# Performance work log

Measured on AMD Instinct MI355X. Metric: run time of the kernel, lower is better.

The kernel has to match this reference:

```python
import jax, jax.numpy as jnp
import numpy as np

N_NODES = 100000
N_EDGES = 1600000
IN = 128
HID = 128
EPS = 1e-5


def setup_inputs() -> dict:
    key = jax.random.key(0)
    ks = jax.random.split(key, 20)
    def lin(k, fi, fo):
        return jax.random.normal(k, (fi, fo), dtype=jnp.float32) / np.sqrt(fi)
    inp = {
        'x': jax.random.normal(ks[0], (N_NODES, IN), dtype=jnp.float32),
        'src': jax.random.randint(ks[1], (N_EDGES,), 0, N_NODES),
        'dst': jax.random.randint(ks[2], (N_EDGES,), 0, N_NODES),
        # SAGEConv layer 1..3: fc_self, fc_neigh, bias
        'Wself1': lin(ks[3], IN, HID), 'Wneigh1': lin(ks[4], IN, HID), 'b1': jnp.zeros((HID,), jnp.float32),
        'Wself2': lin(ks[5], HID, HID), 'Wneigh2': lin(ks[6], HID, HID), 'b2': jnp.zeros((HID,), jnp.float32),
        'Wself3': lin(ks[7], HID, HID), 'Wneigh3': lin(ks[8], HID, HID), 'b3': jnp.zeros((HID,), jnp.float32),
        # shared BatchNorm1d(hid)
        'gamma': jnp.ones((HID,), jnp.float32), 'beta': jnp.zeros((HID,), jnp.float32),
        # decoder MLP hid->hid->hid->1
        'Wd1': lin(ks[9], HID, HID), 'bd1': jnp.zeros((HID,), jnp.float32),
        'Wd2': lin(ks[10], HID, HID), 'bd2': jnp.zeros((HID,), jnp.float32),
        'Wd3': lin(ks[11], HID, 1), 'bd3': jnp.zeros((1,), jnp.float32),
    }
    return inp


def _sage_conv(h, src, dst, deg, Wself, Wneigh, b, n):
    # mean aggregation over in-neighbors: gather + segment-sum + divide
    neigh_sum = jax.ops.segment_sum(h[src], dst, num_segments=n)  # [N, F]
    neigh_mean = neigh_sum / deg[:, None]
    return h @ Wself + neigh_mean @ Wneigh + b


def _batch_norm(h, gamma, beta):
    mu = jnp.mean(h, axis=0)
    var = jnp.mean(jnp.square(h - mu), axis=0)  # biased var, as torch BN training
    return gamma * (h - mu) * jax.lax.rsqrt(var + EPS) + beta


def reference(x, src, dst, Wself1, Wneigh1, b1, Wself2, Wneigh2, b2,
              Wself3, Wneigh3, b3, gamma, beta, Wd1, bd1, Wd2, bd2, Wd3, bd3):
    n = x.shape[0]
    deg = jax.ops.segment_sum(jnp.ones_like(dst, dtype=x.dtype), dst, num_segments=n)
    deg = jnp.maximum(deg, 1.0)
    h = _sage_conv(x, src, dst, deg, Wself1, Wneigh1, b1, n)
    h = jax.nn.relu(_batch_norm(h, gamma, beta))  # dropout = identity (eval)
    h = _sage_conv(h, src, dst, deg, Wself2, Wneigh2, b2, n)
    h = jax.nn.relu(_batch_norm(h, gamma, beta))
    h = _sage_conv(h, src, dst, deg, Wself3, Wneigh3, b3, n)
    # decoder MLP
    h = jax.nn.relu(h @ Wd1 + bd1)
    h = jax.nn.relu(h @ Wd2 + bd2)
    return h @ Wd3 + bd3  # [N, 1]
```

## Files before the change

### kernel.cpp

```cpp
#include <hip/hip_runtime.h>

typedef unsigned short u16;
typedef unsigned int u32;
using bf16x8 = __attribute__((ext_vector_type(8))) __bf16;
using f32x4  = __attribute__((ext_vector_type(4))) float;

#define CAP 48

__global__ void SAGE_79328045957727_kernel() {}

__device__ __forceinline__ float bf2f(u16 u) {
  union { u32 i; float f; } v; v.i = ((u32)u) << 16; return v.f;
}
__device__ __forceinline__ u16 f2bf(float f) {
  union { float f; u32 i; } v; v.f = f;
  u32 x = v.i;
  return (u16)((x + 0x7FFFu + ((x >> 16) & 1u)) >> 16);
}


__global__ void zero_kernel(int* p, int n) {
  int i = blockIdx.x * 256 + threadIdx.x;
  if (i < n) p[i] = 0;
}


__global__ __launch_bounds__(256) void build_kernel(
    const int* __restrict__ src, const int* __restrict__ dst,
    int* __restrict__ deg, int* __restrict__ csr, int E, int npart,
    const float* __restrict__ x, u16* __restrict__ xb, long nelem4,
    const float* w0, const float* w1, const float* w2, const float* w3,
    const float* w4, const float* w5, const float* w6, const float* w7,
    u16* __restrict__ wt) {
  int b = blockIdx.x;
  if (b < 1024) {
    int p = b & 7;
    int brank = b >> 3;
    int lo = p * npart, hi = lo + npart;
    for (int i = brank * 256 + threadIdx.x; i < E; i += 128 * 256) {
      int dv = dst[i];
      if (dv >= lo && dv < hi) {
        int pos = atomicAdd(&deg[dv], 1);
        if (pos < CAP) csr[(size_t)dv * CAP + pos] = src[i];
      }
    }
  } else if (b < 1280) {
    long t = (long)(b - 1024) * 256 + threadIdx.x;
    for (long i4 = t; i4 < nelem4; i4 += 256 * 256) {
      float4 v = ((const float4*)x)[i4];
      u32* op = (u32*)(xb + i4 * 4);
      op[0] = ((u32)f2bf(v.y) << 16) | (u32)f2bf(v.x);
      op[1] = ((u32)f2bf(v.w) << 16) | (u32)f2bf(v.z);
    }
  } else {
    int tg = (b - 1280) * 256 + threadIdx.x;
    for (int k = 0; k < 8; ++k) {
      int idx = tg + k * 16384;
      int m = idx >> 14;
      int i = idx & 16383;
      const float* W = m == 0 ? w0 : m == 1 ? w1 : m == 2 ? w2 : m == 3 ? w3
                     : m == 4 ? w4 : m == 5 ? w5 : m == 6 ? w6 : w7;
      int r = i >> 7, c = i & 127;
      wt[(size_t)m * 16384 + (size_t)c * 128 + r] = f2bf(W[i]);
    }
  }
}


template <int BNIN>
__global__ __launch_bounds__(256) void gather_mean_kernel(
    const u16* __restrict__ H, const int* __restrict__ csr,
    const int* __restrict__ deg, const float* __restrict__ stats,
    const float* __restrict__ gamma, const float* __restrict__ beta,
    u16* __restrict__ M, int N, float invN) {
  __shared__ float sSc[128], sSh[128];
  if (BNIN) {
    int t = threadIdx.x;
    if (t < 128) {
      float mu = stats[t] * invN;
      float var = stats[128 + t] * invN - mu * mu;
      float is = rsqrtf(var + 1e-5f);
      float sc = gamma[t] * is;
      sSc[t] = sc;
      sSh[t] = beta[t] - mu * sc;
    }
    __syncthreads();
  }
  int node = blockIdx.x * 16 + (threadIdx.x >> 4);
  if (node >= N) return;
  int lane = threadIdx.x & 15;
  int fo = lane * 8;
  float sc[8], sh[8];
  if (BNIN) {
    for (int j = 0; j < 8; ++j) { sc[j] = sSc[fo + j]; sh[j] = sSh[fo + j]; }
  }
  const int* nl = csr + (size_t)node * CAP;
  int d = deg[node];
  int dm = d < CAP ? d : CAP;
  float a0=0.f,a1=0.f,a2=0.f,a3=0.f,a4=0.f,a5=0.f,a6=0.f,a7=0.f;

#define ACCQ(q) do { \
    float e0 = bf2f((u16)((q).x & 0xffffu)), e1 = bf2f((u16)((q).x >> 16)); \
    float e2 = bf2f((u16)((q).y & 0xffffu)), e3 = bf2f((u16)((q).y >> 16)); \
    float e4 = bf2f((u16)((q).z & 0xffffu)), e5 = bf2f((u16)((q).z >> 16)); \
    float e6 = bf2f((u16)((q).w & 0xffffu)), e7 = bf2f((u16)((q).w >> 16)); \
    if (BNIN) { \
      e0 = fmaxf(sc[0]*e0+sh[0], 0.f); e1 = fmaxf(sc[1]*e1+sh[1], 0.f); \
      e2 = fmaxf(sc[2]*e2+sh[2], 0.f); e3 = fmaxf(sc[3]*e3+sh[3], 0.f); \
      e4 = fmaxf(sc[4]*e4+sh[4], 0.f); e5 = fmaxf(sc[5]*e5+sh[5], 0.f); \
      e6 = fmaxf(sc[6]*e6+sh[6], 0.f); e7 = fmaxf(sc[7]*e7+sh[7], 0.f); \
    } \
    a0 += e0; a1 += e1; a2 += e2; a3 += e3; \
    a4 += e4; a5 += e5; a6 += e6; a7 += e7; \
  } while (0)

  int e = 0;
  for (; e + 4 <= dm; e += 4) {
    int i0 = nl[e], i1 = nl[e + 1], i2 = nl[e + 2], i3 = nl[e + 3];
    uint4 q0 = *(const uint4*)(H + (size_t)i0 * 128 + fo);
    uint4 q1 = *(const uint4*)(H + (size_t)i1 * 128 + fo);
    uint4 q2 = *(const uint4*)(H + (size_t)i2 * 128 + fo);
    uint4 q3 = *(const uint4*)(H + (size_t)i3 * 128 + fo);
    ACCQ(q0); ACCQ(q1); ACCQ(q2); ACCQ(q3);
  }
  for (; e < dm; ++e) {
    uint4 q = *(const uint4*)(H + (size_t)nl[e] * 128 + fo);
    ACCQ(q);
  }
#undef ACCQ
  float inv = 1.f / (float)(d > 0 ? d : 1);
  uint4 o;
  o.x = ((u32)f2bf(a1 * inv) << 16) | (u32)f2bf(a0 * inv);
  o.y = ((u32)f2bf(a3 * inv) << 16) | (u32)f2bf(a2 * inv);
  o.z = ((u32)f2bf(a5 * inv) << 16) | (u32)f2bf(a4 * inv);
  o.w = ((u32)f2bf(a7 * inv) << 16) | (u32)f2bf(a6 * inv);
  *(uint4*)(M + (size_t)node * 128 + fo) = o;
}


#define LDSROW 136

template <int DUAL, int RELU, int STATS, int BNIN, int FINAL>
__global__ __launch_bounds__(256) void gemm_mfma(
    const u16* __restrict__ A, const u16* __restrict__ B,
    const u16* __restrict__ W1t, const u16* __restrict__ W2t,
    const float* __restrict__ bias, u16* __restrict__ C,
    float* __restrict__ statsOut, const float* __restrict__ statsIn,
    const float* __restrict__ gamma, const float* __restrict__ beta,
    const float* __restrict__ wd3, const float* __restrict__ bd3,
    float* __restrict__ outF, int N, float invN) {
  __shared__ u16 sT[128 * LDSROW];
  __shared__ float sSc[128], sSh[128];
  __shared__ float sOut[128];

  int tid = threadIdx.x;
  int wave = tid >> 6;
  int lane = tid & 63;
  int l15 = lane & 15;
  int quad = lane >> 4;
  size_t row0 = (size_t)blockIdx.x * 128;

  if (BNIN || FINAL) {
    if (tid < 128) {
      if (BNIN) {
        float mu = statsIn[tid] * invN;
        float var = statsIn[128 + tid] * invN - mu * mu;
        float is = rsqrtf(var + 1e-5f);
        float sc = gamma[tid] * is;
        sSc[tid] = sc;
        sSh[tid] = beta[tid] - mu * sc;
      }
      if (FINAL) sOut[tid] = 0.f;
    }
    __syncthreads();
  }

  float bsc[8], bsh[8];
  int cbase = ((tid * 4) & 63) * 2;
  if (BNIN) {
    for (int j = 0; j < 8; ++j) { bsc[j] = sSc[cbase + j]; bsh[j] = sSh[cbase + j]; }
  }

  f32x4 acc[8][2];
  for (int rt = 0; rt < 8; ++rt)
    for (int ct = 0; ct < 2; ++ct)
      for (int i = 0; i < 4; ++i) acc[rt][ct][i] = 0.f;

  bf16x8 wf[2][4];

  for (int ph = 0; ph < (DUAL ? 2 : 1); ++ph) {
    const u16* Asrc = ph ? B : A;
    const u16* Wt = ph ? W2t : W1t;

    for (int ct = 0; ct < 2; ++ct) {
      int col = wave * 32 + ct * 16 + l15;
      for (int kk = 0; kk < 4; ++kk)
        wf[ct][kk] = *(const bf16x8*)(Wt + (size_t)col * 128 + kk * 32 + quad * 8);
    }

    if (ph) __syncthreads();
    for (int j = 0; j < 8; ++j) {
      int idx = j * 1024 + tid * 4;
      int r = idx >> 6;
      int c = idx & 63;
      size_t grow = row0 + r;
      if (grow >= (size_t)N) grow = (size_t)(N - 1);
      const u32* gp = (const u32*)(Asrc + grow * 128) + c;
      u32 v0 = gp[0], v1 = gp[1], v2 = gp[2], v3 = gp[3];
      if (BNIN && ph == 0) {
        float e0 = fmaxf(bsc[0]*bf2f((u16)(v0 & 0xffffu))+bsh[0], 0.f);
        float e1 = fmaxf(bsc[1]*bf2f((u16)(v0 >> 16))+bsh[1], 0.f);
        float e2 = fmaxf(bsc[2]*bf2f((u16)(v1 & 0xffffu))+bsh[2], 0.f);
        float e3 = fmaxf(bsc[3]*bf2f((u16)(v1 >> 16))+bsh[3], 0.f);
        float e4 = fmaxf(bsc[4]*bf2f((u16)(v2 & 0xffffu))+bsh[4], 0.f);
        float e5 = fmaxf(bsc[5]*bf2f((u16)(v2 >> 16))+bsh[5], 0.f);
        float e6 = fmaxf(bsc[6]*bf2f((u16)(v3 & 0xffffu))+bsh[6], 0.f);
        float e7 = fmaxf(bsc[7]*bf2f((u16)(v3 >> 16))+bsh[7], 0.f);
        v0 = ((u32)f2bf(e1) << 16) | (u32)f2bf(e0);
        v1 = ((u32)f2bf(e3) << 16) | (u32)f2bf(e2);
        v2 = ((u32)f2bf(e5) << 16) | (u32)f2bf(e4);
        v3 = ((u32)f2bf(e7) << 16) | (u32)f2bf(e6);
      }
      u32* lp = (u32*)(sT + (size_t)r * LDSROW + c * 2);
      lp[0] = v0; lp[1] = v1; lp[2] = v2; lp[3] = v3;
    }
    __syncthreads();

    for (int kk = 0; kk < 4; ++kk) {
      int kbase = kk * 32 + quad * 8;
      for (int rt = 0; rt < 8; ++rt) {
        bf16x8 af = *(const bf16x8*)(sT + (size_t)(rt * 16 + l15) * LDSROW + kbase);
        acc[rt][0] = __builtin_amdgcn_mfma_f32_16x16x32_bf16(af, wf[0][kk], acc[rt][0], 0, 0, 0);
        acc[rt][1] = __builtin_amdgcn_mfma_f32_16x16x32_bf16(af, wf[1][kk], acc[rt][1], 0, 0, 0);
      }
    }
  }

  if (FINAL) {
    int col0 = wave * 32 + l15;
    float bv0 = bias[col0], bv1 = bias[col0 + 16];
    float w30 = wd3[col0], w31 = wd3[col0 + 16];
    for (int rt = 0; rt < 8; ++rt) {
      for (int i = 0; i < 4; ++i) {
        size_t row = row0 + rt * 16 + quad * 4 + i;
        float v0 = fmaxf(acc[rt][0][i] + bv0, 0.f);
        float v1 = fmaxf(acc[rt][1][i] + bv1, 0.f);
        float pv = v0 * w30 + v1 * w31;
        pv += __shfl_xor(pv, 1);
        pv += __shfl_xor(pv, 2);
        pv += __shfl_xor(pv, 4);
        pv += __shfl_xor(pv, 8);
        if (l15 == 0 && row < (size_t)N)
          atomicAdd(&sOut[rt * 16 + quad * 4 + i], pv);
      }
    }
    __syncthreads();
    if (tid < 128) {
      size_t row = row0 + tid;
      if (row < (size_t)N) outF[row] = sOut[tid] + bd3[0];
    }
    return;
  }

  for (int ct = 0; ct < 2; ++ct) {
    int col = wave * 32 + ct * 16 + l15;
    float bv = bias[col];
    float ssum = 0.f, ssq = 0.f;
    for (int rt = 0; rt < 8; ++rt) {
      for (int i = 0; i < 4; ++i) {
        size_t row = row0 + rt * 16 + quad * 4 + i;
        if (row < (size_t)N) {
          float v = acc[rt][ct][i] + bv;
          if (RELU) v = fmaxf(v, 0.f);
          C[row * 128 + col] = f2bf(v);
          if (STATS) { ssum += v; ssq += v * v; }
        }
      }
    }
    if (STATS) {
      for (int o = 16; o < 64; o <<= 1) {
        ssum += __shfl_xor(ssum, o);
        ssq  += __shfl_xor(ssq, o);
      }
      if (quad == 0) {
        atomicAdd(&statsOut[col], ssum);
        atomicAdd(&statsOut[128 + col], ssq);
      }
    }
  }
}


extern "C" void kernel_launch(void* const* d_in, const int* in_sizes, int n_in,
                              void* d_out, int out_size, void* d_ws, size_t ws_size,
                              hipStream_t stream) {
  const float* x      = (const float*)d_in[0];
  const int*   src    = (const int*)d_in[1];
  const int*   dst    = (const int*)d_in[2];
  const float* Wself1 = (const float*)d_in[3];
  const float* Wneigh1= (const float*)d_in[4];
  const float* b1     = (const float*)d_in[5];
  const float* Wself2 = (const float*)d_in[6];
  const float* Wneigh2= (const float*)d_in[7];
  const float* b2     = (const float*)d_in[8];
  const float* Wself3 = (const float*)d_in[9];
  const float* Wneigh3= (const float*)d_in[10];
  const float* b3     = (const float*)d_in[11];
  const float* gamma  = (const float*)d_in[12];
  const float* beta   = (const float*)d_in[13];
  const float* Wd1    = (const float*)d_in[14];
  const float* bd1    = (const float*)d_in[15];
  const float* Wd2    = (const float*)d_in[16];
  const float* bd2    = (const float*)d_in[17];
  const float* Wd3    = (const float*)d_in[18];
  const float* bd3    = (const float*)d_in[19];
  float* out = (float*)d_out;

  int N = in_sizes[0] / 128;
  int E = in_sizes[1];
  int npart = (N + 7) / 8;

  char* ws = (char*)d_ws;
  size_t off = 0;
  int* deg; int* csr; float* stats1; float* stats2;
  u16* xb; u16* ZA; u16* ZB; u16* M; u16* wt;
  deg   = (int*)(ws + off);   off += (size_t)N * 4;
  stats1= (float*)(ws + off); off += 256 * 4;
  stats2= (float*)(ws + off); off += 256 * 4;
  off = (off + 511) & ~(size_t)511;
  csr  = (int*)(ws + off);   off += ((size_t)N * CAP * 4 + 511) & ~(size_t)511;
  wt   = (u16*)(ws + off);   off += ((size_t)8 * 16384 * 2 + 511) & ~(size_t)511;
  xb   = (u16*)(ws + off);   off += ((size_t)N * 128 * 2 + 511) & ~(size_t)511;
  ZA   = (u16*)(ws + off);   off += ((size_t)N * 128 * 2 + 511) & ~(size_t)511;
  ZB   = (u16*)(ws + off);   off += ((size_t)N * 128 * 2 + 511) & ~(size_t)511;
  M    = (u16*)(ws + off);   off += ((size_t)N * 128 * 2 + 511) & ~(size_t)511;

  u16* wtS1 = wt + 0 * 16384; u16* wtN1 = wt + 1 * 16384;
  u16* wtS2 = wt + 2 * 16384; u16* wtN2 = wt + 3 * 16384;
  u16* wtS3 = wt + 4 * 16384; u16* wtN3 = wt + 5 * 16384;
  u16* wtD1 = wt + 6 * 16384; u16* wtD2 = wt + 7 * 16384;

  zero_kernel<<<(N + 512 + 255) / 256, 256, 0, stream>>>(deg, N + 512);

  long nelem4 = (long)N * 128 / 4;
  build_kernel<<<1344, 256, 0, stream>>>(
      src, dst, deg, csr, E, npart, x, xb, nelem4,
      Wself1, Wneigh1, Wself2, Wneigh2, Wself3, Wneigh3, Wd1, Wd2, wt);

  int strips = (N + 127) / 128;
  int g16    = (N + 15) / 16;
  float invN = 1.f / (float)N;

  gather_mean_kernel<0><<<g16, 256, 0, stream>>>(
      xb, csr, deg, (const float*)0, (const float*)0, (const float*)0, M, N, invN);
  gemm_mfma<1, 0, 1, 0, 0><<<strips, 256, 0, stream>>>(
      xb, M, wtS1, wtN1, b1, ZA, stats1, (const float*)0, (const float*)0,
      (const float*)0, (const float*)0, (const float*)0, (float*)0, N, invN);

  gather_mean_kernel<1><<<g16, 256, 0, stream>>>(
      ZA, csr, deg, stats1, gamma, beta, M, N, invN);
  gemm_mfma<1, 0, 1, 1, 0><<<strips, 256, 0, stream>>>(
      ZA, M, wtS2, wtN2, b2, ZB, stats2, stats1, gamma, beta,
      (const float*)0, (const float*)0, (float*)0, N, invN);

  gather_mean_kernel<1><<<g16, 256, 0, stream>>>(
      ZB, csr, deg, stats2, gamma, beta, M, N, invN);
  gemm_mfma<1, 0, 0, 1, 0><<<strips, 256, 0, stream>>>(
      ZB, M, wtS3, wtN3, b3, ZA, (float*)0, stats2, gamma, beta,
      (const float*)0, (const float*)0, (float*)0, N, invN);

  gemm_mfma<0, 1, 0, 0, 0><<<strips, 256, 0, stream>>>(
      ZA, (const u16*)0, wtD1, (const u16*)0, bd1, ZB, (float*)0, (const float*)0,
      (const float*)0, (const float*)0, (const float*)0, (const float*)0, (float*)0, N, invN);
  gemm_mfma<0, 1, 0, 0, 1><<<strips, 256, 0, stream>>>(
      ZB, (const u16*)0, wtD2, (const u16*)0, bd2, (u16*)0, (float*)0, (const float*)0,
      (const float*)0, (const float*)0, Wd3, bd3, out, N, invN);
}
```

Before: 598.1 us.

## Fuse layer-3 SAGE GEMM with decoder MLP into one kernel

Merges the third SAGEConv GEMM and the two decoder GEMMs plus the final dot product into a single kernel that keeps each 128-row tile in LDS and registers between stages. This removes two kernel launches and the global write and read of two N x 128 bf16 intermediates. The fused kernel is longer and serialises three GEMM stages per block with extra barriers. The generic GEMM template is trimmed to the dual, stats-producing variant only.

```diff
diff --git a/kernel.cpp b/kernel.cpp
--- a/kernel.cpp
+++ b/kernel.cpp
@@ -140,18 +140,16 @@
 
 #define LDSROW 136
 
-template <int DUAL, int RELU, int STATS, int BNIN, int FINAL>
+template <int BNIN>
 __global__ __launch_bounds__(256) void gemm_mfma(
     const u16* __restrict__ A, const u16* __restrict__ B,
     const u16* __restrict__ W1t, const u16* __restrict__ W2t,
     const float* __restrict__ bias, u16* __restrict__ C,
     float* __restrict__ statsOut, const float* __restrict__ statsIn,
     const float* __restrict__ gamma, const float* __restrict__ beta,
-    const float* __restrict__ wd3, const float* __restrict__ bd3,
-    float* __restrict__ outF, int N, float invN) {
+    int N, float invN) {
   __shared__ u16 sT[128 * LDSROW];
   __shared__ float sSc[128], sSh[128];
-  __shared__ float sOut[128];
 
   int tid = threadIdx.x;
   int wave = tid >> 6;
@@ -160,17 +158,14 @@
   int quad = lane >> 4;
   size_t row0 = (size_t)blockIdx.x * 128;
 
-  if (BNIN || FINAL) {
+  if (BNIN) {
     if (tid < 128) {
-      if (BNIN) {
-        float mu = statsIn[tid] * invN;
-        float var = statsIn[128 + tid] * invN - mu * mu;
-        float is = rsqrtf(var + 1e-5f);
-        float sc = gamma[tid] * is;
-        sSc[tid] = sc;
-        sSh[tid] = beta[tid] - mu * sc;
-      }
-      if (FINAL) sOut[tid] = 0.f;
+      float mu = statsIn[tid] * invN;
+      float var = statsIn[128 + tid] * invN - mu * mu;
+      float is = rsqrtf(var + 1e-5f);
+      float sc = gamma[tid] * is;
+      sSc[tid] = sc;
+      sSh[tid] = beta[tid] - mu * sc;
     }
     __syncthreads();
   }
@@ -188,7 +183,7 @@
 
   bf16x8 wf[2][4];
 
-  for (int ph = 0; ph < (DUAL ? 2 : 1); ++ph) {
+  for (int ph = 0; ph < 2; ++ph) {
     const u16* Asrc = ph ? B : A;
     const u16* Wt = ph ? W2t : W1t;
 
@@ -236,9 +231,164 @@
     }
   }
 
-  if (FINAL) {
+  for (int ct = 0; ct < 2; ++ct) {
+    int col = wave * 32 + ct * 16 + l15;
+    float bv = bias[col];
+    float ssum = 0.f, ssq = 0.f;
+    for (int rt = 0; rt < 8; ++rt) {
+      for (int i = 0; i < 4; ++i) {
+        size_t row = row0 + rt * 16 + quad * 4 + i;
+        if (row < (size_t)N) {
+          float v = acc[rt][ct][i] + bv;
+          C[row * 128 + col] = f2bf(v);
+          ssum += v; ssq += v * v;
+        }
+      }
+    }
+    for (int o = 16; o < 64; o <<= 1) {
+      ssum += __shfl_xor(ssum, o);
+      ssq  += __shfl_xor(ssq, o);
+    }
+    if (quad == 0) {
+      atomicAdd(&statsOut[col], ssum);
+      atomicAdd(&statsOut[128 + col], ssq);
+    }
+  }
+}
+
+
+__global__ __launch_bounds__(256) void megagemm(
+    const u16* __restrict__ ZB, const u16* __restrict__ M,
+    const u16* __restrict__ wtS3, const u16* __restrict__ wtN3,
+    const float* __restrict__ b3,
+    const u16* __restrict__ wtD1, const float* __restrict__ bd1,
+    const u16* __restrict__ wtD2, const float* __restrict__ bd2,
+    const float* __restrict__ wd3, const float* __restrict__ bd3,
+    const float* __restrict__ statsIn, const float* __restrict__ gamma,
+    const float* __restrict__ beta,
+    float* __restrict__ outF, int N, float invN) {
+  __shared__ u16 sT[128 * LDSROW];
+  __shared__ float sSc[128], sSh[128];
+  __shared__ float sOut[128];
+
+  int tid = threadIdx.x;
+  int wave = tid >> 6;
+  int lane = tid & 63;
+  int l15 = lane & 15;
+  int quad = lane >> 4;
+  size_t row0 = (size_t)blockIdx.x * 128;
+
+  if (tid < 128) {
+    float mu = statsIn[tid] * invN;
+    float var = statsIn[128 + tid] * invN - mu * mu;
+    float is = rsqrtf(var + 1e-5f);
+    float sc = gamma[tid] * is;
+    sSc[tid] = sc;
+    sSh[tid] = beta[tid] - mu * sc;
+    sOut[tid] = 0.f;
+  }
+  __syncthreads();
+
+  float bsc[8], bsh[8];
+  int cbase = ((tid * 4) & 63) * 2;
+  for (int j = 0; j < 8; ++j) { bsc[j] = sSc[cbase + j]; bsh[j] = sSh[cbase + j]; }
+
+  f32x4 acc[8][2];
+  for (int rt = 0; rt < 8; ++rt)
+    for (int ct = 0; ct < 2; ++ct)
+      for (int i = 0; i < 4; ++i) acc[rt][ct][i] = 0.f;
+
+  bf16x8 wf[2][4];
+
+  for (int ph = 0; ph < 2; ++ph) {
+    const u16* Asrc = ph ? M : ZB;
+    const u16* Wt = ph ? wtN3 : wtS3;
+
+    for (int ct = 0; ct < 2; ++ct) {
+      int col = wave * 32 + ct * 16 + l15;
+      for (int kk = 0; kk < 4; ++kk)
+        wf[ct][kk] = *(const bf16x8*)(Wt + (size_t)col * 128 + kk * 32 + quad * 8);
+    }
+
+    if (ph) __syncthreads();
+    for (int j = 0; j < 8; ++j) {
+      int idx = j * 1024 + tid * 4;
+      int r = idx >> 6;
+      int c = idx & 63;
+      size_t grow = row0 + r;
+      if (grow >= (size_t)N) grow = (size_t)(N - 1);
+      const u32* gp = (const u32*)(Asrc + grow * 128) + c;
+      u32 v0 = gp[0], v1 = gp[1], v2 = gp[2], v3 = gp[3];
+      if (ph == 0) {
+        float e0 = fmaxf(bsc[0]*bf2f((u16)(v0 & 0xffffu))+bsh[0], 0.f);
+        float e1 = fmaxf(bsc[1]*bf2f((u16)(v0 >> 16))+bsh[1], 0.f);
+        float e2 = fmaxf(bsc[2]*bf2f((u16)(v1 & 0xffffu))+bsh[2], 0.f);
+        float e3 = fmaxf(bsc[3]*bf2f((u16)(v1 >> 16))+bsh[3], 0.f);
+        float e4 = fmaxf(bsc[4]*bf2f((u16)(v2 & 0xffffu))+bsh[4], 0.f);
+        float e5 = fmaxf(bsc[5]*bf2f((u16)(v2 >> 16))+bsh[5], 0.f);
+        float e6 = fmaxf(bsc[6]*bf2f((u16)(v3 & 0xffffu))+bsh[6], 0.f);
+        float e7 = fmaxf(bsc[7]*bf2f((u16)(v3 >> 16))+bsh[7], 0.f);
+        v0 = ((u32)f2bf(e1) << 16) | (u32)f2bf(e0);
+        v1 = ((u32)f2bf(e3) << 16) | (u32)f2bf(e2);
+        v2 = ((u32)f2bf(e5) << 16) | (u32)f2bf(e4);
+        v3 = ((u32)f2bf(e7) << 16) | (u32)f2bf(e6);
+      }
+      u32* lp = (u32*)(sT + (size_t)r * LDSROW + c * 2);
+      lp[0] = v0; lp[1] = v1; lp[2] = v2; lp[3] = v3;
+    }
+    __syncthreads();
+
+    for (int kk = 0; kk < 4; ++kk) {
+      int kbase = kk * 32 + quad * 8;
+      for (int rt = 0; rt < 8; ++rt) {
+        bf16x8 af = *(const bf16x8*)(sT + (size_t)(rt * 16 + l15) * LDSROW + kbase);
+        acc[rt][0] = __builtin_amdgcn_mfma_f32_16x16x32_bf16(af, wf[0][kk], acc[rt][0], 0, 0, 0);
+        acc[rt][1] = __builtin_amdgcn_mfma_f32_16x16x32_bf16(af, wf[1][kk], acc[rt][1], 0, 0, 0);
+      }
+    }
+  }
+
+  for (int g = 0; g < 2; ++g) {
+    const u16* Wt = g ? wtD2 : wtD1;
+    const float* bs = g ? bd1 : b3;
+    int do_relu = g;
+
+    __syncthreads();
+    for (int ct = 0; ct < 2; ++ct) {
+      int col = wave * 32 + ct * 16 + l15;
+      float bv = bs[col];
+      for (int rt = 0; rt < 8; ++rt) {
+        for (int i = 0; i < 4; ++i) {
+          int row = rt * 16 + quad * 4 + i;
+          float v = acc[rt][ct][i] + bv;
+          if (do_relu) v = fmaxf(v, 0.f);
+          sT[(size_t)row * LDSROW + col] = f2bf(v);
+        }
+      }
+    }
+    __syncthreads();
+
+    for (int ct = 0; ct < 2; ++ct) {
+      int col = wave * 32 + ct * 16 + l15;
+      for (int kk = 0; kk < 4; ++kk)
+        wf[ct][kk] = *(const bf16x8*)(Wt + (size_t)col * 128 + kk * 32 + quad * 8);
+    }
+    for (int rt = 0; rt < 8; ++rt)
+      for (int ct = 0; ct < 2; ++ct)
+        for (int i = 0; i < 4; ++i) acc[rt][ct][i] = 0.f;
+    for (int kk = 0; kk < 4; ++kk) {
+      int kbase = kk * 32 + quad * 8;
+      for (int rt = 0; rt < 8; ++rt) {
+        bf16x8 af = *(const bf16x8*)(sT + (size_t)(rt * 16 + l15) * LDSROW + kbase);
+        acc[rt][0] = __builtin_amdgcn_mfma_f32_16x16x32_bf16(af, wf[0][kk], acc[rt][0], 0, 0, 0);
+        acc[rt][1] = __builtin_amdgcn_mfma_f32_16x16x32_bf16(af, wf[1][kk], acc[rt][1], 0, 0, 0);
+      }
+    }
+  }
+
+  {
     int col0 = wave * 32 + l15;
-    float bv0 = bias[col0], bv1 = bias[col0 + 16];
+    float bv0 = bd2[col0], bv1 = bd2[col0 + 16];
     float w30 = wd3[col0], w31 = wd3[col0 + 16];
     for (int rt = 0; rt < 8; ++rt) {
       for (int i = 0; i < 4; ++i) {
@@ -258,34 +408,6 @@
     if (tid < 128) {
       size_t row = row0 + tid;
       if (row < (size_t)N) outF[row] = sOut[tid] + bd3[0];
-    }
-    return;
-  }
-
-  for (int ct = 0; ct < 2; ++ct) {
-    int col = wave * 32 + ct * 16 + l15;
-    float bv = bias[col];
-    float ssum = 0.f, ssq = 0.f;
-    for (int rt = 0; rt < 8; ++rt) {
-      for (int i = 0; i < 4; ++i) {
-        size_t row = row0 + rt * 16 + quad * 4 + i;
-        if (row < (size_t)N) {
-          float v = acc[rt][ct][i] + bv;
-          if (RELU) v = fmaxf(v, 0.f);
-          C[row * 128 + col] = f2bf(v);
-          if (STATS) { ssum += v; ssq += v * v; }
-        }
-      }
-    }
-    if (STATS) {
-      for (int o = 16; o < 64; o <<= 1) {
-        ssum += __shfl_xor(ssum, o);
-        ssq  += __shfl_xor(ssq, o);
-      }
-      if (quad == 0) {
-        atomicAdd(&statsOut[col], ssum);
-        atomicAdd(&statsOut[128 + col], ssq);
-      }
     }
   }
 }
@@ -353,26 +475,18 @@
 
   gather_mean_kernel<0><<<g16, 256, 0, stream>>>(
       xb, csr, deg, (const float*)0, (const float*)0, (const float*)0, M, N, invN);
-  gemm_mfma<1, 0, 1, 0, 0><<<strips, 256, 0, stream>>>(
+  gemm_mfma<0><<<strips, 256, 0, stream>>>(
       xb, M, wtS1, wtN1, b1, ZA, stats1, (const float*)0, (const float*)0,
-      (const float*)0, (const float*)0, (const float*)0, (float*)0, N, invN);
+      (const float*)0, N, invN);
 
   gather_mean_kernel<1><<<g16, 256, 0, stream>>>(
       ZA, csr, deg, stats1, gamma, beta, M, N, invN);
-  gemm_mfma<1, 0, 1, 1, 0><<<strips, 256, 0, stream>>>(
-      ZA, M, wtS2, wtN2, b2, ZB, stats2, stats1, gamma, beta,
-      (const float*)0, (const float*)0, (float*)0, N, invN);
+  gemm_mfma<1><<<strips, 256, 0, stream>>>(
+      ZA, M, wtS2, wtN2, b2, ZB, stats2, stats1, gamma, beta, N, invN);
 
   gather_mean_kernel<1><<<g16, 256, 0, stream>>>(
       ZB, csr, deg, stats2, gamma, beta, M, N, invN);
-  gemm_mfma<1, 0, 0, 1, 0><<<strips, 256, 0, stream>>>(
-      ZB, M, wtS3, wtN3, b3, ZA, (float*)0, stats2, gamma, beta,
-      (const float*)0, (const float*)0, (float*)0, N, invN);
-
-  gemm_mfma<0, 1, 0, 0, 0><<<strips, 256, 0, stream>>>(
-      ZA, (const u16*)0, wtD1, (const u16*)0, bd1, ZB, (float*)0, (const float*)0,
-      (const float*)0, (const float*)0, (const float*)0, (const float*)0, (float*)0, N, invN);
-  gemm_mfma<0, 1, 0, 0, 1><<<strips, 256, 0, stream>>>(
-      ZB, (const u16*)0, wtD2, (const u16*)0, bd2, (u16*)0, (float*)0, (const float*)0,
-      (const float*)0, (const float*)0, Wd3, bd3, out, N, invN);
-}
+  megagemm<<<strips, 256, 0, stream>>>(
+      ZB, M, wtS3, wtN3, b3, wtD1, bd1, wtD2, bd2, Wd3, bd3,
+      stats2, gamma, beta, out, N, invN);
+}
```

Result: faster. 541.0 us (-9.6%).
